# Performance work log

Measured on AMD Instinct MI355X. Metric: run time of the kernel, lower is better.

Reference implementation:

```python
import jax, jax.numpy as jnp
import numpy as np

B, I, O, P = 32, 2048, 64, 4  # batch, input caps, output caps, pose side
D = P * P
EPS = 1e-7
N_ITERS = 3

def setup_inputs() -> dict:
    key = jax.random.key(0)
    k1, k2, k3, k4, k5 = jax.random.split(key, 5)
    return {
        'input_poses': jax.random.normal(k1, (B, I, P, P), dtype=jnp.float32),
        'input_activations': jax.random.uniform(k2, (B, I), dtype=jnp.float32),
        'w': jax.random.normal(k3, (O, I, P, P), dtype=jnp.float32) * 0.05,
        'beta_a': jax.random.normal(k4, (1, O), dtype=jnp.float32),
        'beta_u': jax.random.normal(k5, (1, O), dtype=jnp.float32),
    }

def em_routing(V, a_in, beta_a, beta_u):
    # V: [B,O,I,D] votes, a_in: [B,I], beta_a/beta_u: [1,O]
    b, o, i, d = V.shape
    R = jnp.full((b, o, i), 1.0 / o, dtype=V.dtype)
    mu = None
    a_out = None
    for t in range(N_ITERS):
        inv_temp = 1.0 + t  # inverse temperature (lambda) schedule
        # ---- M-step ----
        r = R * a_in[:, None, :]                              # [B,O,I]
        r_sum = r.sum(axis=2, keepdims=True) + EPS            # [B,O,1]
        mu = jnp.einsum('boi,boid->bod', r, V) / r_sum        # [B,O,D]
        diff2 = (V - mu[:, :, None, :]) ** 2                  # [B,O,I,D]
        sigma2 = jnp.einsum('boi,boid->bod', r, diff2) / r_sum + EPS
        cost = (beta_u[:, :, None] + 0.5 * jnp.log(sigma2)) * r_sum  # [B,O,D]
        a_out = jax.nn.sigmoid(inv_temp * (beta_a - cost.sum(axis=-1)))  # [B,O]
        # ---- E-step ----
        if t < N_ITERS - 1:
            log_p = -0.5 * jnp.sum(diff2 / sigma2[:, :, None, :] + jnp.log(sigma2)[:, :, None, :], axis=-1)  # [B,O,I]
            R = jax.nn.softmax(jnp.log(a_out + EPS)[:, :, None] + log_p, axis=1)
    return mu, a_out

def reference(input_poses, input_activations, w, beta_a, beta_u):
    # votes: poses[B,1,I,P,P] @ w[O,I,P,P] -> [B,O,I,P,P]
    votes = jnp.einsum('bipq,oiqr->boipr', input_poses, w)
    V = votes.reshape(B, O, I, D)
    mu, a_out = em_routing(V, input_activations, beta_a, beta_u)
    capsule_poses = mu.reshape(B, O, P, P)
    return capsule_poses, a_out
```

## Files before the change

kernel.cpp:

```cpp
#include <hip/hip_runtime.h>
#include <stdint.h>

constexpr int Bn = 32, In = 2048;
constexpr float EPSF = 1e-7f;
constexpr int NC  = 32;
constexpr int IPB = In / NC;
constexpr int IPW = IPB / 4;

template <int CTRL>
__device__ __forceinline__ float dpp_add(float x) {
  int y = __builtin_amdgcn_update_dpp(0, __float_as_int(x), CTRL, 0xF, 0xF, true);
  return x + __int_as_float(y);
}

__device__ __forceinline__ float wave_sum64(float x) {
  x = dpp_add<0x121>(x);
  x = dpp_add<0x122>(x);
  x = dpp_add<0x124>(x);
  x = dpp_add<0x128>(x);
#if __has_builtin(__builtin_amdgcn_permlane16_swap)
  {
    auto pr = __builtin_amdgcn_permlane16_swap(__float_as_uint(x), __float_as_uint(x), false, false);
    x = __uint_as_float(pr[0]) + __uint_as_float(pr[1]);
  }
#else
  x += __int_as_float(__builtin_amdgcn_ds_swizzle(__float_as_int(x), 0x401F));
#endif
#if __has_builtin(__builtin_amdgcn_permlane32_swap)
  {
    auto pr = __builtin_amdgcn_permlane32_swap(__float_as_uint(x), __float_as_uint(x), false, false);
    x = __uint_as_float(pr[0]) + __uint_as_float(pr[1]);
  }
#else
  x += __shfl_xor(x, 32);
#endif
  return x;
}

__global__ __launch_bounds__(256) void transpose_w_k(const float4* __restrict__ w,
                                                     float4* __restrict__ w_t) {
  int idx = blockIdx.x * 256 + threadIdx.x;
  int o = idx >> 13;
  int rest = idx & 8191;
  int i = rest >> 2;
  int k = rest & 3;
  w_t[(size_t)((i << 2) + k) * 64 + o] = w[idx];
}

template <int TPASS>
__global__ __launch_bounds__(256, 2) void pass_k(const float* __restrict__ poses,
                                                 const float* __restrict__ a_in,
                                                 const float* __restrict__ w_t,
                                                 const float* __restrict__ params,
                                                 float* __restrict__ partials) {
  const int gid = blockIdx.x;
  const int xcd = gid & 7;
  const int s   = gid >> 3;
  const int b   = s & 31;
  const int cc  = xcd * 4 + (s >> 5);
  const int tid = threadIdx.x, wv = tid >> 6, ln = tid & 63;
  const int i0 = __builtin_amdgcn_readfirstlane(cc * IPB + wv * IPW);

  float mu[16], hs[16], c0 = 0.f;
  if (TPASS > 0) {
    const float4* pp4 = (const float4*)(params + (size_t)(b * 64 + ln) * 36);
#pragma unroll
    for (int k = 0; k < 4; ++k) {
      float4 v = pp4[k];
      mu[4 * k] = v.x; mu[4 * k + 1] = v.y; mu[4 * k + 2] = v.z; mu[4 * k + 3] = v.w;
    }
#pragma unroll
    for (int k = 0; k < 4; ++k) {
      float4 v = pp4[4 + k];
      hs[4 * k] = v.x; hs[4 * k + 1] = v.y; hs[4 * k + 2] = v.z; hs[4 * k + 3] = v.w;
    }
    c0 = ((const float*)pp4)[32];
  }

  float rs = 0.f, S1[16], S2[16];
#pragma unroll
  for (int d = 0; d < 16; ++d) { S1[d] = 0.f; S2[d] = 0.f; }

  const float4* wt4 = (const float4*)w_t;
  const float* pbase = poses + ((size_t)b * In + i0) * 16;
  const float* abase = a_in + (size_t)b * In + i0;

#pragma unroll 4
  for (int ii = 0; ii < IPW; ++ii) {
    const int i = i0 + ii;
    float4 w0 = wt4[(size_t)(i * 4 + 0) * 64 + ln];
    float4 w1 = wt4[(size_t)(i * 4 + 1) * 64 + ln];
    float4 w2 = wt4[(size_t)(i * 4 + 2) * 64 + ln];
    float4 w3 = wt4[(size_t)(i * 4 + 3) * 64 + ln];
    const float4* pp = (const float4*)(pbase + ii * 16);
    float4 p0 = pp[0], p1 = pp[1], p2 = pp[2], p3 = pp[3];
    float V[16];
#define VROW(p, Pv)                                                              \
    V[p * 4 + 0] = fmaf(Pv.w, w3.x, fmaf(Pv.z, w2.x, fmaf(Pv.y, w1.x, Pv.x * w0.x))); \
    V[p * 4 + 1] = fmaf(Pv.w, w3.y, fmaf(Pv.z, w2.y, fmaf(Pv.y, w1.y, Pv.x * w0.y))); \
    V[p * 4 + 2] = fmaf(Pv.w, w3.z, fmaf(Pv.z, w2.z, fmaf(Pv.y, w1.z, Pv.x * w0.z))); \
    V[p * 4 + 3] = fmaf(Pv.w, w3.w, fmaf(Pv.z, w2.w, fmaf(Pv.y, w1.w, Pv.x * w0.w)));
    VROW(0, p0) VROW(1, p1) VROW(2, p2) VROW(3, p3)
#undef VROW
    const float a = abase[ii];
    float r;
    if (TPASS == 0) {
      r = a * 0.015625f;
    } else {
      float u0 = c0, u1 = 0.f, u2 = 0.f, u3 = 0.f;
#pragma unroll
      for (int j = 0; j < 4; ++j) {
        float d0 = V[j] - mu[j];           u0 = fmaf(-d0 * d0, hs[j], u0);
        float d1 = V[4 + j] - mu[4 + j];   u1 = fmaf(-d1 * d1, hs[4 + j], u1);
        float d2 = V[8 + j] - mu[8 + j];   u2 = fmaf(-d2 * d2, hs[8 + j], u2);
        float d3 = V[12 + j] - mu[12 + j]; u3 = fmaf(-d3 * d3, hs[12 + j], u3);
      }
      float u = (u0 + u1) + (u2 + u3);
      float e = __expf(u);
      float ss = wave_sum64(e) + 1e-37f;
      r = a * e * __builtin_amdgcn_rcpf(ss);
    }
    rs += r;
#pragma unroll
    for (int d = 0; d < 16; ++d) {
      float t1 = r * V[d];
      S1[d] += t1;
      S2[d] = fmaf(t1, V[d], S2[d]);
    }
  }

  __shared__ float lds[4][33][64];
  lds[wv][0][ln] = rs;
#pragma unroll
  for (int d = 0; d < 16; ++d) {
    lds[wv][1 + d][ln] = S1[d];
    lds[wv][17 + d][ln] = S2[d];
  }
  __syncthreads();
  for (int idx = tid; idx < 33 * 64; idx += 256) {
    int j = idx >> 6, o = idx & 63;
    float ssum = lds[0][j][o] + lds[1][j][o] + lds[2][j][o] + lds[3][j][o];
    partials[((size_t)(b * NC + cc) * 33 + j) * 64 + o] = ssum;
  }
}

__global__ __launch_bounds__(256) void red_k(const float* __restrict__ partials,
                                             float* __restrict__ red) {
  const int idx = blockIdx.x * 256 + threadIdx.x;
  const int b = idx / 2112;
  const int rr = idx - b * 2112;
  const float* base = partials + (size_t)b * NC * 2112 + rr;
  float s = 0.f;
#pragma unroll 8
  for (int c = 0; c < NC; ++c) s += base[(size_t)c * 2112];
  red[idx] = s;
}

template <int TPASS>
__global__ __launch_bounds__(256) void fin_k(const float* __restrict__ red,
                                             const float* __restrict__ beta_a,
                                             const float* __restrict__ beta_u,
                                             float* __restrict__ params,
                                             float* __restrict__ out) {
  const int g = blockIdx.x * 256 + threadIdx.x;
  const int b = g >> 6, o = g & 63;
  const float* base = red + (size_t)b * 2112 + o;
  const float r_sum = base[0] + EPSF;
  const float inv = 1.f / r_sum;
  float muv[16], sg[16], lsum = 0.f;
#pragma unroll
  for (int d = 0; d < 16; ++d) {
    float m = base[(1 + d) * 64] * inv;
    float s2 = fmaxf(base[(17 + d) * 64] * inv - m * m, 0.f) + EPSF;
    muv[d] = m; sg[d] = s2; lsum += logf(s2);
  }
  const float cost = (16.f * beta_u[o] + 0.5f * lsum) * r_sum;
  const float aout = 1.f / (1.f + __expf(-(float)(TPASS + 1) * (beta_a[o] - cost)));
  if (TPASS < 2) {
    float c0 = logf(aout + EPSF) - 0.5f * lsum;
    float mx = c0;
#pragma unroll
    for (int k = 1; k < 64; k <<= 1) mx = fmaxf(mx, __shfl_xor(mx, k));
    float* pp = params + (size_t)g * 36;
#pragma unroll
    for (int d = 0; d < 16; ++d) {
      pp[d] = muv[d];
      pp[16 + d] = 0.5f / sg[d];
    }
    pp[32] = c0 - mx;
  } else {
#pragma unroll
    for (int d = 0; d < 16; ++d) out[(size_t)g * 16 + d] = muv[d];
    out[Bn * 64 * 16 + g] = aout;
  }
}

extern "C" void kernel_launch(void* const* d_in, const int* in_sizes, int n_in,
                              void* d_out, int out_size, void* d_ws, size_t ws_size,
                              hipStream_t stream) {
  const float* poses  = (const float*)d_in[0];
  const float* a_in   = (const float*)d_in[1];
  const float* w      = (const float*)d_in[2];
  const float* beta_a = (const float*)d_in[3];
  const float* beta_u = (const float*)d_in[4];
  float* out = (float*)d_out;

  float* w_t      = (float*)d_ws;
  float* partials = w_t + (size_t)In * 64 * 16;
  float* red      = partials + (size_t)Bn * NC * 33 * 64;
  float* params   = red + (size_t)Bn * 33 * 64;

  transpose_w_k<<<dim3(In * 64 * 4 / 256), 256, 0, stream>>>((const float4*)w, (float4*)w_t);

  dim3 pg(Bn * NC);
  dim3 rg(Bn * 33 * 64 / 256);
  pass_k<0><<<pg, 256, 0, stream>>>(poses, a_in, w_t, params, partials);
  red_k<<<rg, 256, 0, stream>>>(partials, red);
  fin_k<0><<<Bn * 64 / 256, 256, 0, stream>>>(red, beta_a, beta_u, params, out);
  pass_k<1><<<pg, 256, 0, stream>>>(poses, a_in, w_t, params, partials);
  red_k<<<rg, 256, 0, stream>>>(partials, red);
  fin_k<1><<<Bn * 64 / 256, 256, 0, stream>>>(red, beta_a, beta_u, params, out);
  pass_k<2><<<pg, 256, 0, stream>>>(poses, a_in, w_t, params, partials);
  red_k<<<rg, 256, 0, stream>>>(partials, red);
  fin_k<2><<<Bn * 64 / 256, 256, 0, stream>>>(red, beta_a, beta_u, params, out);
}
```

Before: 161.2 us.

## Fuse reduction into finalize, expand quadratic log-prob, prefetch weights, raise occupancy

Merges the separate cross-chunk reduction kernel into the finalize kernel, which now uses one block per batch and an LDS buffer, removing three launches and the intermediate buffer round trip. In the pass kernel the Gaussian exponent is expanded into precomputed k0/k1/k2 coefficients applied to V and V², reusing V² for the S2 accumulation. Next-iteration weight loads are software-prefetched. The waves-per-EU hint is raised to 4. The finalize kernel now has far fewer blocks (32), so its reduction is less parallel. The expanded quadratic form may lose floating-point precision through cancellation.

```diff
diff --git a/kernel.cpp b/kernel.cpp
--- a/kernel.cpp
+++ b/kernel.cpp
@@ -48,11 +48,13 @@
 }
 
 template <int TPASS>
-__global__ __launch_bounds__(256, 2) void pass_k(const float* __restrict__ poses,
-                                                 const float* __restrict__ a_in,
-                                                 const float* __restrict__ w_t,
-                                                 const float* __restrict__ params,
-                                                 float* __restrict__ partials) {
+__global__ __launch_bounds__(256)
+__attribute__((amdgpu_waves_per_eu(4, 4)))
+void pass_k(const float* __restrict__ poses,
+            const float* __restrict__ a_in,
+            const float* __restrict__ w_t,
+            const float* __restrict__ params,
+            float* __restrict__ partials) {
   const int gid = blockIdx.x;
   const int xcd = gid & 7;
   const int s   = gid >> 3;
@@ -61,9 +63,10 @@
   const int tid = threadIdx.x, wv = tid >> 6, ln = tid & 63;
   const int i0 = __builtin_amdgcn_readfirstlane(cc * IPB + wv * IPW);
 
-  float mu[16], hs[16], c0 = 0.f;
+  float k0 = 0.f, k1[16], k2[16];
   if (TPASS > 0) {
     const float4* pp4 = (const float4*)(params + (size_t)(b * 64 + ln) * 36);
+    float mu[16];
 #pragma unroll
     for (int k = 0; k < 4; ++k) {
       float4 v = pp4[k];
@@ -72,9 +75,14 @@
 #pragma unroll
     for (int k = 0; k < 4; ++k) {
       float4 v = pp4[4 + k];
-      hs[4 * k] = v.x; hs[4 * k + 1] = v.y; hs[4 * k + 2] = v.z; hs[4 * k + 3] = v.w;
-    }
-    c0 = ((const float*)pp4)[32];
+      k2[4 * k] = v.x; k2[4 * k + 1] = v.y; k2[4 * k + 2] = v.z; k2[4 * k + 3] = v.w;
+    }
+    k0 = ((const float*)pp4)[32];
+#pragma unroll
+    for (int d = 0; d < 16; ++d) {
+      k1[d] = 2.f * k2[d] * mu[d];
+      k0 = fmaf(-k2[d], mu[d] * mu[d], k0);
+    }
   }
 
   float rs = 0.f, S1[16], S2[16];
@@ -85,35 +93,44 @@
   const float* pbase = poses + ((size_t)b * In + i0) * 16;
   const float* abase = a_in + (size_t)b * In + i0;
 
+  float4 cw0 = wt4[(size_t)(i0 * 4 + 0) * 64 + ln];
+  float4 cw1 = wt4[(size_t)(i0 * 4 + 1) * 64 + ln];
+  float4 cw2 = wt4[(size_t)(i0 * 4 + 2) * 64 + ln];
+  float4 cw3 = wt4[(size_t)(i0 * 4 + 3) * 64 + ln];
+
 #pragma unroll 4
   for (int ii = 0; ii < IPW; ++ii) {
-    const int i = i0 + ii;
-    float4 w0 = wt4[(size_t)(i * 4 + 0) * 64 + ln];
-    float4 w1 = wt4[(size_t)(i * 4 + 1) * 64 + ln];
-    float4 w2 = wt4[(size_t)(i * 4 + 2) * 64 + ln];
-    float4 w3 = wt4[(size_t)(i * 4 + 3) * 64 + ln];
+    const int inx = (ii + 1 < IPW) ? (i0 + ii + 1) : (i0 + ii);
+    float4 nw0 = wt4[(size_t)(inx * 4 + 0) * 64 + ln];
+    float4 nw1 = wt4[(size_t)(inx * 4 + 1) * 64 + ln];
+    float4 nw2 = wt4[(size_t)(inx * 4 + 2) * 64 + ln];
+    float4 nw3 = wt4[(size_t)(inx * 4 + 3) * 64 + ln];
+
     const float4* pp = (const float4*)(pbase + ii * 16);
     float4 p0 = pp[0], p1 = pp[1], p2 = pp[2], p3 = pp[3];
-    float V[16];
-#define VROW(p, Pv)                                                              \
-    V[p * 4 + 0] = fmaf(Pv.w, w3.x, fmaf(Pv.z, w2.x, fmaf(Pv.y, w1.x, Pv.x * w0.x))); \
-    V[p * 4 + 1] = fmaf(Pv.w, w3.y, fmaf(Pv.z, w2.y, fmaf(Pv.y, w1.y, Pv.x * w0.y))); \
-    V[p * 4 + 2] = fmaf(Pv.w, w3.z, fmaf(Pv.z, w2.z, fmaf(Pv.y, w1.z, Pv.x * w0.z))); \
-    V[p * 4 + 3] = fmaf(Pv.w, w3.w, fmaf(Pv.z, w2.w, fmaf(Pv.y, w1.w, Pv.x * w0.w)));
+    float V[16], q[16];
+#define VROW(p, Pv)                                                                    \
+    V[p * 4 + 0] = fmaf(Pv.w, cw3.x, fmaf(Pv.z, cw2.x, fmaf(Pv.y, cw1.x, Pv.x * cw0.x))); \
+    V[p * 4 + 1] = fmaf(Pv.w, cw3.y, fmaf(Pv.z, cw2.y, fmaf(Pv.y, cw1.y, Pv.x * cw0.y))); \
+    V[p * 4 + 2] = fmaf(Pv.w, cw3.z, fmaf(Pv.z, cw2.z, fmaf(Pv.y, cw1.z, Pv.x * cw0.z))); \
+    V[p * 4 + 3] = fmaf(Pv.w, cw3.w, fmaf(Pv.z, cw2.w, fmaf(Pv.y, cw1.w, Pv.x * cw0.w)));
     VROW(0, p0) VROW(1, p1) VROW(2, p2) VROW(3, p3)
 #undef VROW
+#pragma unroll
+    for (int d = 0; d < 16; ++d) q[d] = V[d] * V[d];
+
     const float a = abase[ii];
     float r;
     if (TPASS == 0) {
       r = a * 0.015625f;
     } else {
-      float u0 = c0, u1 = 0.f, u2 = 0.f, u3 = 0.f;
+      float u0 = k0, u1 = 0.f, u2 = 0.f, u3 = 0.f;
 #pragma unroll
       for (int j = 0; j < 4; ++j) {
-        float d0 = V[j] - mu[j];           u0 = fmaf(-d0 * d0, hs[j], u0);
-        float d1 = V[4 + j] - mu[4 + j];   u1 = fmaf(-d1 * d1, hs[4 + j], u1);
-        float d2 = V[8 + j] - mu[8 + j];   u2 = fmaf(-d2 * d2, hs[8 + j], u2);
-        float d3 = V[12 + j] - mu[12 + j]; u3 = fmaf(-d3 * d3, hs[12 + j], u3);
+        u0 = fmaf(-k2[j], q[j], fmaf(k1[j], V[j], u0));
+        u1 = fmaf(-k2[4 + j], q[4 + j], fmaf(k1[4 + j], V[4 + j], u1));
+        u2 = fmaf(-k2[8 + j], q[8 + j], fmaf(k1[8 + j], V[8 + j], u2));
+        u3 = fmaf(-k2[12 + j], q[12 + j], fmaf(k1[12 + j], V[12 + j], u3));
       }
       float u = (u0 + u1) + (u2 + u3);
       float e = __expf(u);
@@ -123,10 +140,10 @@
     rs += r;
 #pragma unroll
     for (int d = 0; d < 16; ++d) {
-      float t1 = r * V[d];
-      S1[d] += t1;
-      S2[d] = fmaf(t1, V[d], S2[d]);
-    }
+      S1[d] = fmaf(r, V[d], S1[d]);
+      S2[d] = fmaf(r, q[d], S2[d]);
+    }
+    cw0 = nw0; cw1 = nw1; cw2 = nw2; cw3 = nw3;
   }
 
   __shared__ float lds[4][33][64];
@@ -144,54 +161,54 @@
   }
 }
 
-__global__ __launch_bounds__(256) void red_k(const float* __restrict__ partials,
-                                             float* __restrict__ red) {
-  const int idx = blockIdx.x * 256 + threadIdx.x;
-  const int b = idx / 2112;
-  const int rr = idx - b * 2112;
-  const float* base = partials + (size_t)b * NC * 2112 + rr;
-  float s = 0.f;
-#pragma unroll 8
-  for (int c = 0; c < NC; ++c) s += base[(size_t)c * 2112];
-  red[idx] = s;
-}
-
 template <int TPASS>
-__global__ __launch_bounds__(256) void fin_k(const float* __restrict__ red,
+__global__ __launch_bounds__(256) void fin_k(const float* __restrict__ partials,
                                              const float* __restrict__ beta_a,
                                              const float* __restrict__ beta_u,
                                              float* __restrict__ params,
                                              float* __restrict__ out) {
-  const int g = blockIdx.x * 256 + threadIdx.x;
-  const int b = g >> 6, o = g & 63;
-  const float* base = red + (size_t)b * 2112 + o;
-  const float r_sum = base[0] + EPSF;
-  const float inv = 1.f / r_sum;
-  float muv[16], sg[16], lsum = 0.f;
-#pragma unroll
-  for (int d = 0; d < 16; ++d) {
-    float m = base[(1 + d) * 64] * inv;
-    float s2 = fmaxf(base[(17 + d) * 64] * inv - m * m, 0.f) + EPSF;
-    muv[d] = m; sg[d] = s2; lsum += logf(s2);
-  }
-  const float cost = (16.f * beta_u[o] + 0.5f * lsum) * r_sum;
-  const float aout = 1.f / (1.f + __expf(-(float)(TPASS + 1) * (beta_a[o] - cost)));
-  if (TPASS < 2) {
-    float c0 = logf(aout + EPSF) - 0.5f * lsum;
-    float mx = c0;
-#pragma unroll
-    for (int k = 1; k < 64; k <<= 1) mx = fmaxf(mx, __shfl_xor(mx, k));
-    float* pp = params + (size_t)g * 36;
+  const int b = blockIdx.x;
+  const int tid = threadIdx.x;
+  __shared__ float redL[33 * 64];
+  for (int idx = tid; idx < 33 * 64; idx += 256) {
+    const float* base = partials + (size_t)b * NC * 2112 + idx;
+    float s = 0.f;
+#pragma unroll 8
+    for (int c = 0; c < NC; ++c) s += base[(size_t)c * 2112];
+    redL[idx] = s;
+  }
+  __syncthreads();
+  if (tid < 64) {
+    const int o = tid;
+    const float r_sum = redL[o] + EPSF;
+    const float inv = 1.f / r_sum;
+    float muv[16], sg[16], lsum = 0.f;
 #pragma unroll
     for (int d = 0; d < 16; ++d) {
-      pp[d] = muv[d];
-      pp[16 + d] = 0.5f / sg[d];
-    }
-    pp[32] = c0 - mx;
-  } else {
-#pragma unroll
-    for (int d = 0; d < 16; ++d) out[(size_t)g * 16 + d] = muv[d];
-    out[Bn * 64 * 16 + g] = aout;
+      float m = redL[(1 + d) * 64 + o] * inv;
+      float s2 = fmaxf(redL[(17 + d) * 64 + o] * inv - m * m, 0.f) + EPSF;
+      muv[d] = m; sg[d] = s2; lsum += logf(s2);
+    }
+    const float cost = (16.f * beta_u[o] + 0.5f * lsum) * r_sum;
+    const float aout = 1.f / (1.f + __expf(-(float)(TPASS + 1) * (beta_a[o] - cost)));
+    if (TPASS < 2) {
+      float c0 = logf(aout + EPSF) - 0.5f * lsum;
+      float mx = c0;
+#pragma unroll
+      for (int k = 1; k < 64; k <<= 1) mx = fmaxf(mx, __shfl_xor(mx, k));
+      float* pp = params + (size_t)(b * 64 + o) * 36;
+#pragma unroll
+      for (int d = 0; d < 16; ++d) {
+        pp[d] = muv[d];
+        pp[16 + d] = 0.5f / sg[d];
+      }
+      pp[32] = c0 - mx;
+    } else {
+      const int g = b * 64 + o;
+#pragma unroll
+      for (int d = 0; d < 16; ++d) out[(size_t)g * 16 + d] = muv[d];
+      out[Bn * 64 * 16 + g] = aout;
+    }
   }
 }
 
@@ -207,20 +224,15 @@
 
   float* w_t      = (float*)d_ws;
   float* partials = w_t + (size_t)In * 64 * 16;
-  float* red      = partials + (size_t)Bn * NC * 33 * 64;
-  float* params   = red + (size_t)Bn * 33 * 64;
+  float* params   = partials + (size_t)Bn * NC * 33 * 64;
 
   transpose_w_k<<<dim3(In * 64 * 4 / 256), 256, 0, stream>>>((const float4*)w, (float4*)w_t);
 
   dim3 pg(Bn * NC);
-  dim3 rg(Bn * 33 * 64 / 256);
   pass_k<0><<<pg, 256, 0, stream>>>(poses, a_in, w_t, params, partials);
-  red_k<<<rg, 256, 0, stream>>>(partials, red);
-  fin_k<0><<<Bn * 64 / 256, 256, 0, stream>>>(red, beta_a, beta_u, params, out);
+  fin_k<0><<<Bn, 256, 0, stream>>>(partials, beta_a, beta_u, params, out);
   pass_k<1><<<pg, 256, 0, stream>>>(poses, a_in, w_t, params, partials);
-  red_k<<<rg, 256, 0, stream>>>(partials, red);
-  fin_k<1><<<Bn * 64 / 256, 256, 0, stream>>>(red, beta_a, beta_u, params, out);
+  fin_k<1><<<Bn, 256, 0, stream>>>(partials, beta_a, beta_u, params, out);
   pass_k<2><<<pg, 256, 0, stream>>>(poses, a_in, w_t, params, partials);
-  red_k<<<rg, 256, 0, stream>>>(partials, red);
-  fin_k<2><<<Bn * 64 / 256, 256, 0, stream>>>(red, beta_a, beta_u, params, out);
-}
+  fin_k<2><<<Bn, 256, 0, stream>>>(partials, beta_a, beta_u, params, out);
+}
```

Result: slower. 194.1 us (+20.4%).
